# Kernel tuning notes

Hardware: AMD Instinct MI355X
Metric: run time of the kernel (lower is better)

## Reference

```python
import jax, jax.numpy as jnp
import numpy as np

B, T = 32, 50
H, D, V = 1024, 512, 50257


def setup_inputs() -> dict:
    key = jax.random.key(0)
    ks = jax.random.split(key, 8)
    s = 0.05  # small init scale to keep LSTM gates in a sane range
    return {
        "inputs": jax.random.normal(ks[0], (B, H), jnp.float32),          # initial hidden state
        "targets": jax.random.randint(ks[1], (B, T), 0, V, jnp.int32),     # teacher-forcing tokens
        "emb": jax.random.normal(ks[2], (V, D), jnp.float32) * s,
        "W_ih": jax.random.normal(ks[3], (4 * H, D), jnp.float32) * s,     # torch gate order i,f,g,o
        "W_hh": jax.random.normal(ks[4], (4 * H, H), jnp.float32) * s,
        "b_ih": jnp.zeros((4 * H,), jnp.float32),
        "b_hh": jnp.zeros((4 * H,), jnp.float32),
        "W_proj": jax.random.normal(ks[5], (V, H), jnp.float32) * s,
        "b_proj": jnp.zeros((V,), jnp.float32),
    }


def reference(inputs, targets, emb, W_ih, W_hh, b_ih, b_hh, W_proj, b_proj):
    b, t = targets.shape
    h = inputs.shape[1]
    # decoder input tokens: BOS(=1) at step 0, then targets shifted right by one
    tok = jnp.concatenate([jnp.ones((b, 1), targets.dtype), targets[:, :-1]], axis=1)  # [B,T]
    x = emb[tok]  # [B,T,D]
    # precompute input contribution to all gates for every step
    xg = jnp.einsum("btd,gd->btg", x, W_ih) + b_ih + b_hh  # [B,T,4H]

    def step(carry, xg_t):
        hs, cs = carry
        g = xg_t + hs @ W_hh.T  # [B,4H]
        i = jax.nn.sigmoid(g[:, :h])
        f = jax.nn.sigmoid(g[:, h:2 * h])
        gg = jnp.tanh(g[:, 2 * h:3 * h])
        o = jax.nn.sigmoid(g[:, 3 * h:])
        cs = f * cs + i * gg
        hs = o * jnp.tanh(cs)
        return (hs, cs), hs

    c0 = jnp.zeros_like(inputs)
    _, hs = jax.lax.scan(step, (inputs, c0), jnp.swapaxes(xg, 0, 1))  # hs: [T,B,H]
    hs = jnp.swapaxes(hs, 0, 1)  # [B,T,H]
    logits = jnp.einsum("bth,vh->btv", hs, W_proj) + b_proj  # [B,T,V]
    predictions = jnp.argmax(logits, axis=-1)  # [B,T]
    return logits, predictions
```

## Files before the change

kernel.cpp:

```cpp
#include <hip/hip_runtime.h>
#include <math.h>

#define BB 32
#define TT 50
#define HH 1024
#define DD 512
#define VV 50257
#define G4H 4096

typedef __attribute__((ext_vector_type(8))) short bf16x8;
typedef __attribute__((ext_vector_type(8))) unsigned short u16x8;
typedef __attribute__((ext_vector_type(4))) float f32x4;

__device__ inline unsigned short f2bf(float x) {
    unsigned u = __float_as_uint(x);
    u = (u + 0x7fff + ((u >> 16) & 1)) >> 16;
    return (unsigned short)u;
}
__device__ inline float bf2f(unsigned short h) {
    return __uint_as_float(((unsigned)h) << 16);
}
__device__ inline void gl16(const void* g, void* l) {
    __builtin_amdgcn_global_load_lds(
        (const __attribute__((address_space(1))) unsigned int*)g,
        (__attribute__((address_space(3))) unsigned int*)l, 16, 0, 0);
}

__global__ void split_f32(const float* __restrict__ x,
                          unsigned short* __restrict__ hi,
                          unsigned short* __restrict__ lo, long n4) {
    long i = (long)blockIdx.x * 256 + threadIdx.x;
    long stride = (long)gridDim.x * 256;
    for (; i < n4; i += stride) {
        float4 v = ((const float4*)x)[i];
        ushort4 h, l;
        h.x = f2bf(v.x); l.x = f2bf(v.x - bf2f(h.x));
        h.y = f2bf(v.y); l.y = f2bf(v.y - bf2f(h.y));
        h.z = f2bf(v.z); l.z = f2bf(v.z - bf2f(h.z));
        h.w = f2bf(v.w); l.w = f2bf(v.w - bf2f(h.w));
        ((ushort4*)hi)[i] = h;
        ((ushort4*)lo)[i] = l;
    }
}

__global__ void xg_gemm(const int* __restrict__ targets,
                        const float* __restrict__ emb,
                        const float* __restrict__ W_ih,
                        const float* __restrict__ b_ih,
                        const float* __restrict__ b_hh,
                        float* __restrict__ xg) {
    __shared__ float As[16][65];
    __shared__ float Bs[16][65];
    const int m0 = blockIdx.y * 64;
    const int n0 = blockIdx.x * 64;
    const int tid = threadIdx.x;
    const int tx = tid & 15;
    const int ty = tid >> 4;
    const int lk = tx;
    const int lm = ty;

    const float* arow[4];
    const float* brow[4];
#pragma unroll
    for (int i = 0; i < 4; i++) {
        int bt = m0 + lm + i * 16;
        int b = bt / TT, t = bt % TT;
        int tok = (t == 0) ? 1 : targets[b * TT + (t - 1)];
        arow[i] = emb + (size_t)tok * DD;
        int n = n0 + lm + i * 16;
        brow[i] = W_ih + (size_t)n * DD;
    }

    float acc[4][4] = {};
    for (int k0 = 0; k0 < DD; k0 += 16) {
#pragma unroll
        for (int i = 0; i < 4; i++) As[lk][lm + i * 16] = arow[i][k0 + lk];
#pragma unroll
        for (int i = 0; i < 4; i++) Bs[lk][lm + i * 16] = brow[i][k0 + lk];
        __syncthreads();
#pragma unroll
        for (int k = 0; k < 16; k++) {
            float a[4], bb[4];
#pragma unroll
            for (int i = 0; i < 4; i++) a[i] = As[k][ty + i * 16];
#pragma unroll
            for (int j = 0; j < 4; j++) bb[j] = Bs[k][tx + j * 16];
#pragma unroll
            for (int i = 0; i < 4; i++)
#pragma unroll
                for (int j = 0; j < 4; j++) acc[i][j] += a[i] * bb[j];
        }
        __syncthreads();
    }
#pragma unroll
    for (int i = 0; i < 4; i++) {
        int m = m0 + ty + i * 16;
#pragma unroll
        for (int j = 0; j < 4; j++) {
            int n = n0 + tx + j * 16;
            xg[(size_t)m * G4H + n] = acc[i][j] + b_ih[n] + b_hh[n];
        }
    }
}

#define NH 16
__global__ __launch_bounds__(256, 2) void lstm_mfma(
    const unsigned short* __restrict__ Wh, const unsigned short* __restrict__ Wl,
    const float* __restrict__ xg,
    const unsigned short* __restrict__ hin_h, const unsigned short* __restrict__ hin_l,
    long hin_stride,
    float* __restrict__ c_buf,
    unsigned short* __restrict__ Ah, unsigned short* __restrict__ Al,
    int t) {
    __shared__ unsigned short sWh[2][64 * 64], sWl[2][64 * 64];
    __shared__ unsigned short sHh[2][32 * 64], sHl[2][32 * 64];
    __shared__ float gbuf[4][32][17];
    const int tid = threadIdx.x;
    const int w = tid >> 6;
    const int l = tid & 63;
    const int lr = l & 15, lk = l >> 4;
    const int nh0 = blockIdx.x * NH;

    const int wrow = tid >> 2;
    const int ws0 = (tid & 3) * 2;
    const int wg = wrow >> 4, wj = wrow & 15;
    const unsigned short* gWh = Wh + (size_t)(wg * HH + nh0 + wj) * HH + ws0 * 8;
    const unsigned short* gWl = Wl + (size_t)(wg * HH + nh0 + wj) * HH + ws0 * 8;
    const int wwb0 = wrow * 64 + ((ws0) ^ (wrow & 7)) * 8;
    const int wwb1 = wrow * 64 + ((ws0 + 1) ^ (wrow & 7)) * 8;

    const int hp = tid & 127;
    const int hrow = hp >> 2;
    const int hs0 = (hp & 3) * 2;
    const unsigned short* gH =
        ((tid < 128) ? hin_h : hin_l) + (size_t)hrow * hin_stride + hs0 * 8;
    const int hsel = (tid < 128) ? 0 : 1;
    const int hwb0 = hrow * 64 + ((hs0) ^ (hrow & 7)) * 8;
    const int hwb1 = hrow * 64 + ((hs0 + 1) ^ (hrow & 7)) * 8;

    f32x4 acc0 = (f32x4){0.f, 0.f, 0.f, 0.f};
    f32x4 acc1 = (f32x4){0.f, 0.f, 0.f, 0.f};

    u16x8 rWh0 = *(const u16x8*)gWh, rWh1 = *(const u16x8*)(gWh + 8);
    u16x8 rWl0 = *(const u16x8*)gWl, rWl1 = *(const u16x8*)(gWl + 8);
    u16x8 rH0  = *(const u16x8*)gH,  rH1  = *(const u16x8*)(gH + 8);
    *(u16x8*)&sWh[0][wwb0] = rWh0; *(u16x8*)&sWh[0][wwb1] = rWh1;
    *(u16x8*)&sWl[0][wwb0] = rWl0; *(u16x8*)&sWl[0][wwb1] = rWl1;
    if (hsel == 0) { *(u16x8*)&sHh[0][hwb0] = rH0; *(u16x8*)&sHh[0][hwb1] = rH1; }
    else           { *(u16x8*)&sHl[0][hwb0] = rH0; *(u16x8*)&sHl[0][hwb1] = rH1; }
    rWh0 = *(const u16x8*)(gWh + 64); rWh1 = *(const u16x8*)(gWh + 64 + 8);
    rWl0 = *(const u16x8*)(gWl + 64); rWl1 = *(const u16x8*)(gWl + 64 + 8);
    rH0  = *(const u16x8*)(gH + 64);  rH1  = *(const u16x8*)(gH + 64 + 8);

    int cur = 0;
#pragma unroll 1
    for (int it = 0; it < 16; it++) {
        __syncthreads();
        if (it < 15) {
            const int nxt = cur ^ 1;
            *(u16x8*)&sWh[nxt][wwb0] = rWh0; *(u16x8*)&sWh[nxt][wwb1] = rWh1;
            *(u16x8*)&sWl[nxt][wwb0] = rWl0; *(u16x8*)&sWl[nxt][wwb1] = rWl1;
            if (hsel == 0) { *(u16x8*)&sHh[nxt][hwb0] = rH0; *(u16x8*)&sHh[nxt][hwb1] = rH1; }
            else           { *(u16x8*)&sHl[nxt][hwb0] = rH0; *(u16x8*)&sHl[nxt][hwb1] = rH1; }
            const int kn = (it < 14) ? (it + 2) * 64 : 0;
            rWh0 = *(const u16x8*)(gWh + kn); rWh1 = *(const u16x8*)(gWh + kn + 8);
            rWl0 = *(const u16x8*)(gWl + kn); rWl1 = *(const u16x8*)(gWl + kn + 8);
            rH0  = *(const u16x8*)(gH + kn);  rH1  = *(const u16x8*)(gH + kn + 8);
        }
#pragma unroll
        for (int kk = 0; kk < 2; kk++) {
            const int rsl = ((kk * 4 + lk) ^ (lr & 7)) * 8;
            bf16x8 bh = *(const bf16x8*)&sWh[cur][(w * 16 + lr) * 64 + rsl];
            bf16x8 bl = *(const bf16x8*)&sWl[cur][(w * 16 + lr) * 64 + rsl];
            bf16x8 a0h = *(const bf16x8*)&sHh[cur][lr * 64 + rsl];
            bf16x8 a1h = *(const bf16x8*)&sHh[cur][(16 + lr) * 64 + rsl];
            bf16x8 a0l = *(const bf16x8*)&sHl[cur][lr * 64 + rsl];
            bf16x8 a1l = *(const bf16x8*)&sHl[cur][(16 + lr) * 64 + rsl];
            acc0 = __builtin_amdgcn_mfma_f32_16x16x32_bf16(a0h, bh, acc0, 0, 0, 0);
            acc0 = __builtin_amdgcn_mfma_f32_16x16x32_bf16(a0h, bl, acc0, 0, 0, 0);
            acc0 = __builtin_amdgcn_mfma_f32_16x16x32_bf16(a0l, bh, acc0, 0, 0, 0);
            acc1 = __builtin_amdgcn_mfma_f32_16x16x32_bf16(a1h, bh, acc1, 0, 0, 0);
            acc1 = __builtin_amdgcn_mfma_f32_16x16x32_bf16(a1h, bl, acc1, 0, 0, 0);
            acc1 = __builtin_amdgcn_mfma_f32_16x16x32_bf16(a1l, bh, acc1, 0, 0, 0);
        }
        cur ^= 1;
    }

    __syncthreads();
#pragma unroll
    for (int r = 0; r < 4; r++) {
        gbuf[w][lk * 4 + r][lr] = acc0[r];
        gbuf[w][16 + lk * 4 + r][lr] = acc1[r];
    }
    __syncthreads();

#pragma unroll
    for (int q = 0; q < 2; q++) {
        int idx = tid + q * 256;
        int b = idx >> 4, j = idx & 15;
        size_t xb = ((size_t)b * TT + t) * G4H + nh0 + j;
        float gi_ = gbuf[0][b][j] + xg[xb];
        float gf_ = gbuf[1][b][j] + xg[xb + HH];
        float gg_ = gbuf[2][b][j] + xg[xb + 2 * HH];
        float go_ = gbuf[3][b][j] + xg[xb + 3 * HH];

        float i_ = 1.f / (1.f + expf(-gi_));
        float f_ = 1.f / (1.f + expf(-gf_));
        float g_ = tanhf(gg_);
        float o_ = 1.f / (1.f + expf(-go_));

        int ci = b * HH + nh0 + j;
        float c_old = (t == 0) ? 0.f : c_buf[ci];
        float c_new = f_ * c_old + i_ * g_;
        float h_new = o_ * tanhf(c_new);
        c_buf[ci] = c_new;

        size_t ho = ((size_t)b * TT + t) * HH + nh0 + j;
        unsigned short hh = f2bf(h_new);
        Ah[ho] = hh;
        Al[ho] = f2bf(h_new - bf2f(hh));
    }
}

__global__ void lstm_step(const float* __restrict__ W_hh,
                          const float* __restrict__ xg,
                          const float* __restrict__ h_prev,
                          float* __restrict__ c_buf,
                          float* __restrict__ h_out,
                          float* __restrict__ hs_all,
                          int t) {
    __shared__ float h_s[32][68];
    __shared__ float w_s[32][68];
    const int tid = threadIdx.x;
    const int b = tid & 31;
    const int jl = tid >> 5;
    const int n0 = blockIdx.x * 8;
    const int n = n0 + jl;

    float acc[4] = {0.f, 0.f, 0.f, 0.f};
    for (int k0 = 0; k0 < HH; k0 += 64) {
#pragma unroll
        for (int i = 0; i < 2; i++) {
            int e = tid + i * 256;
            int r = e >> 4;
            int c = e & 15;
            float4 hv = *(const float4*)&h_prev[r * HH + k0 + c * 4];
            *(float4*)&h_s[r][c * 4] = hv;
            int gi = r >> 3, jj = r & 7;
            float4 wv = *(const float4*)&W_hh[(size_t)(gi * HH + n0 + jj) * HH + k0 + c * 4];
            *(float4*)&w_s[r][c * 4] = wv;
        }
        __syncthreads();
#pragma unroll
        for (int k = 0; k < 64; k += 4) {
            float4 hv = *(const float4*)&h_s[b][k];
            float4 w0 = *(const float4*)&w_s[jl][k];
            float4 w1 = *(const float4*)&w_s[8 + jl][k];
            float4 w2 = *(const float4*)&w_s[16 + jl][k];
            float4 w3 = *(const float4*)&w_s[24 + jl][k];
            acc[0] += hv.x * w0.x + hv.y * w0.y + hv.z * w0.z + hv.w * w0.w;
            acc[1] += hv.x * w1.x + hv.y * w1.y + hv.z * w1.z + hv.w * w1.w;
            acc[2] += hv.x * w2.x + hv.y * w2.y + hv.z * w2.z + hv.w * w2.w;
            acc[3] += hv.x * w3.x + hv.y * w3.y + hv.z * w3.z + hv.w * w3.w;
        }
        __syncthreads();
    }

    const int bt = b * TT + t;
    float gi_ = acc[0] + xg[(size_t)bt * G4H + n];
    float gf_ = acc[1] + xg[(size_t)bt * G4H + HH + n];
    float gg_ = acc[2] + xg[(size_t)bt * G4H + 2 * HH + n];
    float go_ = acc[3] + xg[(size_t)bt * G4H + 3 * HH + n];

    float i_ = 1.f / (1.f + expf(-gi_));
    float f_ = 1.f / (1.f + expf(-gf_));
    float g_ = tanhf(gg_);
    float o_ = 1.f / (1.f + expf(-go_));

    float c_old = (t == 0) ? 0.f : c_buf[b * HH + n];
    float c_new = f_ * c_old + i_ * g_;
    float h_new = o_ * tanhf(c_new);

    c_buf[b * HH + n] = c_new;
    h_out[b * HH + n] = h_new;
    hs_all[(size_t)bt * HH + n] = h_new;
}

__global__ __launch_bounds__(256, 4) void proj_mfma(
    const unsigned short* __restrict__ Ah, const unsigned short* __restrict__ Al,
    const unsigned short* __restrict__ Bh, const unsigned short* __restrict__ Bl,
    const float* __restrict__ b_proj, float* __restrict__ logits) {
    __shared__ __attribute__((aligned(16))) unsigned short sA[2][128 * 32];
    __shared__ __attribute__((aligned(16))) unsigned short sB[2][128 * 32];
    const int tid = threadIdx.x;
    const int w = tid >> 6;
    const int l = tid & 63;
    const int wr = w >> 1, wc = w & 1;
    const int lr = l & 15, lk = l >> 4;

    const int d = blockIdx.x;
    const int xcd = d & 7;
    const int k = d >> 3;
    const int ncnt = (xcd == 0) ? 50 : 49;
    const int nstart = (xcd == 0) ? 0 : 50 + (xcd - 1) * 49;
    if (k >= 13 * ncnt) return;
    const int per4 = 4 * ncnt;
    int s, rr_;
    if (k < per4)          { s = 0; rr_ = k; }
    else if (k < 2 * per4) { s = 1; rr_ = k - per4; }
    else if (k < 3 * per4) { s = 2; rr_ = k - 2 * per4; }
    else                   { s = 3; rr_ = k - 3 * per4; }
    const int ssize = (s == 3) ? 1 : 4;
    const int nloc = rr_ / ssize;
    const int mins = rr_ - nloc * ssize;
    const int m0 = (s * 4 + mins) * 128;
    const int n0 = (nstart + nloc) * 128;

    const unsigned short* garr = (w == 0) ? Ah : (w == 1) ? Al : (w == 2) ? Bh : Bl;
    unsigned short* larr = (w == 0) ? sA[0] : (w == 1) ? sA[1]
                         : (w == 2) ? sB[0] : sB[1];
    const int isA = (w < 2);
    const unsigned short* gsrc[8];
#pragma unroll
    for (int i = 0; i < 8; i++) {
        int r = i * 16 + (l >> 2);
        int sl = (l & 3) ^ ((r >> 1) & 3);
        int g = isA ? (m0 + r) : (n0 + r);
        int gmax = isA ? (BB * TT - 1) : (VV - 1);
        if (g > gmax) g = gmax;
        gsrc[i] = garr + (size_t)g * HH + sl * 8;
    }

    const int rswz = (lk ^ ((lr >> 1) & 3)) * 8;

    f32x4 acc[4][4];
#pragma unroll
    for (int i = 0; i < 4; i++)
#pragma unroll
        for (int j = 0; j < 4; j++) acc[i][j] = (f32x4){0.f, 0.f, 0.f, 0.f};

#pragma unroll 1
    for (int it = 0; it < 32; it++) {
        const int k0v = it * 32;
#pragma unroll
        for (int i = 0; i < 8; i++)
            gl16(gsrc[i] + k0v, larr + i * 512);
        __syncthreads();

        bf16x8 ah[4], al[4], bh[4], bl[4];
#pragma unroll
        for (int i = 0; i < 4; i++) {
            int ra = (wr * 64 + i * 16 + lr) * 32 + rswz;
            ah[i] = *(const bf16x8*)&sA[0][ra];
            al[i] = *(const bf16x8*)&sA[1][ra];
        }
#pragma unroll
        for (int j = 0; j < 4; j++) {
            int rb = (wc * 64 + j * 16 + lr) * 32 + rswz;
            bh[j] = *(const bf16x8*)&sB[0][rb];
            bl[j] = *(const bf16x8*)&sB[1][rb];
        }
#pragma unroll
        for (int i = 0; i < 4; i++)
#pragma unroll
            for (int j = 0; j < 4; j++) {
                acc[i][j] = __builtin_amdgcn_mfma_f32_16x16x32_bf16(ah[i], bh[j], acc[i][j], 0, 0, 0);
                acc[i][j] = __builtin_amdgcn_mfma_f32_16x16x32_bf16(ah[i], bl[j], acc[i][j], 0, 0, 0);
                acc[i][j] = __builtin_amdgcn_mfma_f32_16x16x32_bf16(al[i], bh[j], acc[i][j], 0, 0, 0);
            }
        __syncthreads();
    }

    float* ewave = ((float*)sA) + w * 1024;
    const int nn = n0 + wc * 64 + l;
    const float bpv = b_proj[nn < VV ? nn : VV - 1];
    const bool nok = (nn < VV);
#pragma unroll
    for (int i = 0; i < 4; i++) {
#pragma unroll
        for (int j = 0; j < 4; j++)
#pragma unroll
            for (int r2 = 0; r2 < 4; r2++)
                ewave[(lk * 4 + r2) * 64 + j * 16 + lr] = acc[i][j][r2];
#pragma unroll
        for (int rr = 0; rr < 16; rr++) {
            int m = m0 + wr * 64 + i * 16 + rr;
            float v = ewave[rr * 64 + l] + bpv;
            if (m < BB * TT && nok)
                logits[(size_t)m * VV + nn] = v;
        }
    }
}

__global__ void proj_gemm(const float* __restrict__ hs,
                          const float* __restrict__ W_proj,
                          const float* __restrict__ b_proj,
                          float* __restrict__ logits) {
    __shared__ float As[16][65];
    __shared__ float Bs[16][65];
    const int m0 = blockIdx.y * 64;
    const int n0 = blockIdx.x * 64;
    const int tid = threadIdx.x;
    const int tx = tid & 15;
    const int ty = tid >> 4;
    const int lk = tx;
    const int lm = ty;

    const float* arow[4];
    const float* brow[4];
    bool bval[4];
#pragma unroll
    for (int i = 0; i < 4; i++) {
        arow[i] = hs + (size_t)(m0 + lm + i * 16) * HH;
        int n = n0 + lm + i * 16;
        bval[i] = (n < VV);
        brow[i] = W_proj + (size_t)(bval[i] ? n : 0) * HH;
    }

    float acc[4][4] = {};
    for (int k0 = 0; k0 < HH; k0 += 16) {
#pragma unroll
        for (int i = 0; i < 4; i++) As[lk][lm + i * 16] = arow[i][k0 + lk];
#pragma unroll
        for (int i = 0; i < 4; i++)
            Bs[lk][lm + i * 16] = bval[i] ? brow[i][k0 + lk] : 0.f;
        __syncthreads();
#pragma unroll
        for (int k = 0; k < 16; k++) {
            float a[4], bb[4];
#pragma unroll
            for (int i = 0; i < 4; i++) a[i] = As[k][ty + i * 16];
#pragma unroll
            for (int j = 0; j < 4; j++) bb[j] = Bs[k][tx + j * 16];
#pragma unroll
            for (int i = 0; i < 4; i++)
#pragma unroll
                for (int j = 0; j < 4; j++) acc[i][j] += a[i] * bb[j];
        }
        __syncthreads();
    }
#pragma unroll
    for (int i = 0; i < 4; i++) {
        int m = m0 + ty + i * 16;
#pragma unroll
        for (int j = 0; j < 4; j++) {
            int n = n0 + tx + j * 16;
            if (n < VV)
                logits[(size_t)m * VV + n] = acc[i][j] + b_proj[n];
        }
    }
}

__global__ void argmax_kernel(const float* __restrict__ logits,
                              float* __restrict__ preds) {
    const int bt = blockIdx.x;
    const float* row = logits + (size_t)bt * VV;
    const int tid = threadIdx.x;

    float best = -INFINITY;
    int bidx = 0x7fffffff;
    for (int v = tid; v < VV; v += 256) {
        float x = row[v];
        if (x > best) { best = x; bidx = v; }
    }
    __shared__ float sv[256];
    __shared__ int si[256];
    sv[tid] = best;
    si[tid] = bidx;
    __syncthreads();
    for (int s = 128; s > 0; s >>= 1) {
        if (tid < s) {
            float ov = sv[tid + s];
            int oi = si[tid + s];
            if (ov > sv[tid] || (ov == sv[tid] && oi < si[tid])) {
                sv[tid] = ov;
                si[tid] = oi;
            }
        }
        __syncthreads();
    }
    if (tid == 0) preds[bt] = (float)si[0];
}

extern "C" void kernel_launch(void* const* d_in, const int* in_sizes, int n_in,
                              void* d_out, int out_size, void* d_ws, size_t ws_size,
                              hipStream_t stream) {
    const float* inputs = (const float*)d_in[0];
    const int*   targets = (const int*)d_in[1];
    const float* emb    = (const float*)d_in[2];
    const float* W_ih   = (const float*)d_in[3];
    const float* W_hh   = (const float*)d_in[4];
    const float* b_ih   = (const float*)d_in[5];
    const float* b_hh   = (const float*)d_in[6];
    const float* W_proj = (const float*)d_in[7];
    const float* b_proj = (const float*)d_in[8];

    float* out = (float*)d_out;
    float* logits = out;
    float* preds = out + (size_t)BB * TT * VV;

    float* ws = (float*)d_ws;
    float* xg = ws;
    float* cb = xg + (size_t)BB * TT * G4H;
    unsigned short* Ah = (unsigned short*)(cb + (size_t)BB * HH);
    unsigned short* Al = Ah + (size_t)BB * TT * HH;
    unsigned short* Bh = Al + (size_t)BB * TT * HH;
    unsigned short* Bl = Bh + (size_t)VV * HH;
    char* R = (char*)(Bl + (size_t)VV * HH);

    float* hs = (float*)R;
    float* h0 = hs + (size_t)BB * TT * HH;
    float* h1 = h0 + (size_t)BB * HH;
    unsigned short* Wh = (unsigned short*)R;
    unsigned short* Wl = Wh + (size_t)G4H * HH;
    unsigned short* iah = Wl + (size_t)G4H * HH;
    unsigned short* ial = iah + (size_t)BB * HH;

    size_t base = (char*)R - (char*)d_ws;
    size_t need1 = base + ((size_t)BB * TT * HH + 2 * (size_t)BB * HH) * 4;
    size_t need2 = base + (2 * (size_t)G4H * HH + 2 * (size_t)BB * HH) * 2;
    int mode = (ws_size >= need2) ? 2 : (ws_size >= need1) ? 1 : 0;

    if (mode >= 1) {
        split_f32<<<4096, 256, 0, stream>>>(W_proj, Bh, Bl, (long)VV * HH / 4);
    }
    if (mode == 2) {
        split_f32<<<2048, 256, 0, stream>>>(W_hh, Wh, Wl, (long)G4H * HH / 4);
        split_f32<<<32, 256, 0, stream>>>(inputs, iah, ial, (long)BB * HH / 4);
    }

    xg_gemm<<<dim3(64, 25), 256, 0, stream>>>(targets, emb, W_ih, b_ih, b_hh, xg);

    if (mode == 2) {
        for (int t = 0; t < TT; t++) {
            const unsigned short* hh = (t == 0) ? iah : (Ah + (size_t)(t - 1) * HH);
            const unsigned short* hl = (t == 0) ? ial : (Al + (size_t)(t - 1) * HH);
            long hstride = (t == 0) ? HH : (long)TT * HH;
            lstm_mfma<<<64, 256, 0, stream>>>(Wh, Wl, xg, hh, hl, hstride,
                                              cb, Ah, Al, t);
        }
        proj_mfma<<<5200, 256, 0, stream>>>(Ah, Al, Bh, Bl, b_proj, logits);
    } else {
        for (int t = 0; t < TT; t++) {
            const float* hp = (t == 0) ? inputs : ((t & 1) ? h0 : h1);
            float* ho = (t & 1) ? h1 : h0;
            lstm_step<<<128, 256, 0, stream>>>(W_hh, xg, hp, cb, ho, hs, t);
        }
        if (mode == 1) {
            split_f32<<<1600, 256, 0, stream>>>(hs, Ah, Al, (long)BB * TT * HH / 4);
            proj_mfma<<<5200, 256, 0, stream>>>(Ah, Al, Bh, Bl, b_proj, logits);
        } else {
            proj_gemm<<<dim3(786, 25), 256, 0, stream>>>(hs, W_proj, b_proj, logits);
        }
    }

    argmax_kernel<<<1600, 256, 0, stream>>>(logits, preds);
}
```

Baseline: 1.380 ms.

## Use direct global-to-LDS loads for LSTM recurrent GEMM tiles

Replaces the register-staged double-buffered loads of W_hh (hi/lo bf16) and hidden-state tiles in the per-step LSTM kernel with global_load_lds async copies into a merged, swizzled shared buffer. The swizzle is moved to the global source address so each wave copies contiguous 16-byte chunks per lane. This is meant to cut VGPR pressure and the VALU/LDS-write cost of staging through registers. The per-step kernel is latency-bound, so the gain may be small, and correctness depends on the waits issued around the async LDS writes.

```diff
diff --git a/kernel.cpp b/kernel.cpp
--- a/kernel.cpp
+++ b/kernel.cpp
@@ -112,8 +112,8 @@
     float* __restrict__ c_buf,
     unsigned short* __restrict__ Ah, unsigned short* __restrict__ Al,
     int t) {
-    __shared__ unsigned short sWh[2][64 * 64], sWl[2][64 * 64];
-    __shared__ unsigned short sHh[2][32 * 64], sHl[2][32 * 64];
+    __shared__ __attribute__((aligned(16))) unsigned short sW[2][2][64 * 64];
+    __shared__ __attribute__((aligned(16))) unsigned short sH[2][2][32 * 64];
     __shared__ float gbuf[4][32][17];
     const int tid = threadIdx.x;
     const int w = tid >> 6;
@@ -121,61 +121,65 @@
     const int lr = l & 15, lk = l >> 4;
     const int nh0 = blockIdx.x * NH;
 
-    const int wrow = tid >> 2;
-    const int ws0 = (tid & 3) * 2;
-    const int wg = wrow >> 4, wj = wrow & 15;
-    const unsigned short* gWh = Wh + (size_t)(wg * HH + nh0 + wj) * HH + ws0 * 8;
-    const unsigned short* gWl = Wl + (size_t)(wg * HH + nh0 + wj) * HH + ws0 * 8;
-    const int wwb0 = wrow * 64 + ((ws0) ^ (wrow & 7)) * 8;
-    const int wwb1 = wrow * 64 + ((ws0 + 1) ^ (wrow & 7)) * 8;
-
-    const int hp = tid & 127;
-    const int hrow = hp >> 2;
-    const int hs0 = (hp & 3) * 2;
-    const unsigned short* gH =
-        ((tid < 128) ? hin_h : hin_l) + (size_t)hrow * hin_stride + hs0 * 8;
-    const int hsel = (tid < 128) ? 0 : 1;
-    const int hwb0 = hrow * 64 + ((hs0) ^ (hrow & 7)) * 8;
-    const int hwb1 = hrow * 64 + ((hs0 + 1) ^ (hrow & 7)) * 8;
+    const int rowc = l >> 3;
+    const int p = l & 7;
+    const unsigned short* gsrc[6];
+    unsigned short* lp0[6];
+    unsigned short* lp1[6];
+#pragma unroll
+    for (int i = 0; i < 6; i++) {
+        const int c = w * 6 + i;
+        const int sl = p ^ rowc;
+        if (c < 16) {
+            const int hl = (c >> 3) & 1;
+            const int cc = c & 7;
+            const int r = cc * 8 + rowc;
+            const int wg = r >> 4, wj = r & 15;
+            const unsigned short* base = hl ? Wl : Wh;
+            gsrc[i] = base + (size_t)(wg * HH + nh0 + wj) * HH + sl * 8;
+            lp0[i] = &sW[0][hl][cc * 512];
+            lp1[i] = &sW[1][hl][cc * 512];
+        } else {
+            const int hc = c - 16;
+            const int hl = (hc >> 2) & 1;
+            const int cc = hc & 3;
+            const int r = cc * 8 + rowc;
+            const unsigned short* base = hl ? hin_l : hin_h;
+            gsrc[i] = base + (size_t)r * hin_stride + sl * 8;
+            lp0[i] = &sH[0][hl][cc * 512];
+            lp1[i] = &sH[1][hl][cc * 512];
+        }
+    }
 
     f32x4 acc0 = (f32x4){0.f, 0.f, 0.f, 0.f};
     f32x4 acc1 = (f32x4){0.f, 0.f, 0.f, 0.f};
 
-    u16x8 rWh0 = *(const u16x8*)gWh, rWh1 = *(const u16x8*)(gWh + 8);
-    u16x8 rWl0 = *(const u16x8*)gWl, rWl1 = *(const u16x8*)(gWl + 8);
-    u16x8 rH0  = *(const u16x8*)gH,  rH1  = *(const u16x8*)(gH + 8);
-    *(u16x8*)&sWh[0][wwb0] = rWh0; *(u16x8*)&sWh[0][wwb1] = rWh1;
-    *(u16x8*)&sWl[0][wwb0] = rWl0; *(u16x8*)&sWl[0][wwb1] = rWl1;
-    if (hsel == 0) { *(u16x8*)&sHh[0][hwb0] = rH0; *(u16x8*)&sHh[0][hwb1] = rH1; }
-    else           { *(u16x8*)&sHl[0][hwb0] = rH0; *(u16x8*)&sHl[0][hwb1] = rH1; }
-    rWh0 = *(const u16x8*)(gWh + 64); rWh1 = *(const u16x8*)(gWh + 64 + 8);
-    rWl0 = *(const u16x8*)(gWl + 64); rWl1 = *(const u16x8*)(gWl + 64 + 8);
-    rH0  = *(const u16x8*)(gH + 64);  rH1  = *(const u16x8*)(gH + 64 + 8);
+#pragma unroll
+    for (int i = 0; i < 6; i++) gl16(gsrc[i], lp0[i]);
 
     int cur = 0;
 #pragma unroll 1
     for (int it = 0; it < 16; it++) {
         __syncthreads();
         if (it < 15) {
-            const int nxt = cur ^ 1;
-            *(u16x8*)&sWh[nxt][wwb0] = rWh0; *(u16x8*)&sWh[nxt][wwb1] = rWh1;
-            *(u16x8*)&sWl[nxt][wwb0] = rWl0; *(u16x8*)&sWl[nxt][wwb1] = rWl1;
-            if (hsel == 0) { *(u16x8*)&sHh[nxt][hwb0] = rH0; *(u16x8*)&sHh[nxt][hwb1] = rH1; }
-            else           { *(u16x8*)&sHl[nxt][hwb0] = rH0; *(u16x8*)&sHl[nxt][hwb1] = rH1; }
-            const int kn = (it < 14) ? (it + 2) * 64 : 0;
-            rWh0 = *(const u16x8*)(gWh + kn); rWh1 = *(const u16x8*)(gWh + kn + 8);
-            rWl0 = *(const u16x8*)(gWl + kn); rWl1 = *(const u16x8*)(gWl + kn + 8);
-            rH0  = *(const u16x8*)(gH + kn);  rH1  = *(const u16x8*)(gH + kn + 8);
+            const int kn = (it + 1) * 64;
+            if (cur == 0) {
+#pragma unroll
+                for (int i = 0; i < 6; i++) gl16(gsrc[i] + kn, lp1[i]);
+            } else {
+#pragma unroll
+                for (int i = 0; i < 6; i++) gl16(gsrc[i] + kn, lp0[i]);
+            }
         }
 #pragma unroll
         for (int kk = 0; kk < 2; kk++) {
             const int rsl = ((kk * 4 + lk) ^ (lr & 7)) * 8;
-            bf16x8 bh = *(const bf16x8*)&sWh[cur][(w * 16 + lr) * 64 + rsl];
-            bf16x8 bl = *(const bf16x8*)&sWl[cur][(w * 16 + lr) * 64 + rsl];
-            bf16x8 a0h = *(const bf16x8*)&sHh[cur][lr * 64 + rsl];
-            bf16x8 a1h = *(const bf16x8*)&sHh[cur][(16 + lr) * 64 + rsl];
-            bf16x8 a0l = *(const bf16x8*)&sHl[cur][lr * 64 + rsl];
-            bf16x8 a1l = *(const bf16x8*)&sHl[cur][(16 + lr) * 64 + rsl];
+            bf16x8 bh = *(const bf16x8*)&sW[cur][0][(w * 16 + lr) * 64 + rsl];
+            bf16x8 bl = *(const bf16x8*)&sW[cur][1][(w * 16 + lr) * 64 + rsl];
+            bf16x8 a0h = *(const bf16x8*)&sH[cur][0][lr * 64 + rsl];
+            bf16x8 a1h = *(const bf16x8*)&sH[cur][0][(16 + lr) * 64 + rsl];
+            bf16x8 a0l = *(const bf16x8*)&sH[cur][1][lr * 64 + rsl];
+            bf16x8 a1l = *(const bf16x8*)&sH[cur][1][(16 + lr) * 64 + rsl];
             acc0 = __builtin_amdgcn_mfma_f32_16x16x32_bf16(a0h, bh, acc0, 0, 0, 0);
             acc0 = __builtin_amdgcn_mfma_f32_16x16x32_bf16(a0h, bl, acc0, 0, 0, 0);
             acc0 = __builtin_amdgcn_mfma_f32_16x16x32_bf16(a0l, bh, acc0, 0, 0, 0);
```

Result: slower. 1.461 ms (+5.9%).

## Split LSTM step K-reduction across two wave groups in 512-thread blocks

Applied to the files above, without the earlier changes.

Doubles the lstm_mfma block to 512 threads. Each half of the block handles half of the K=1024 recurrent reduction with its own double-buffered shared tiles, and the partial gate sums are combined through shared memory before the activation epilogue. This halves the serial K-loop length per step, aiming to cut per-launch latency of the 50 sequential recurrent kernels. In exchange it doubles shared memory and the gbuf footprint. The block count stays at 64, so the GPU remains mostly idle.

```diff
diff --git a/kernel.cpp b/kernel.cpp
--- a/kernel.cpp
+++ b/kernel.cpp
@@ -104,7 +104,7 @@
 }
 
 #define NH 16
-__global__ __launch_bounds__(256, 2) void lstm_mfma(
+__global__ __launch_bounds__(512, 2) void lstm_mfma(
     const unsigned short* __restrict__ Wh, const unsigned short* __restrict__ Wl,
     const float* __restrict__ xg,
     const unsigned short* __restrict__ hin_h, const unsigned short* __restrict__ hin_l,
@@ -112,29 +112,35 @@
     float* __restrict__ c_buf,
     unsigned short* __restrict__ Ah, unsigned short* __restrict__ Al,
     int t) {
-    __shared__ unsigned short sWh[2][64 * 64], sWl[2][64 * 64];
-    __shared__ unsigned short sHh[2][32 * 64], sHl[2][32 * 64];
-    __shared__ float gbuf[4][32][17];
+    __shared__ unsigned short sW[2][2][2][64 * 64];
+    __shared__ unsigned short sH[2][2][2][32 * 64];
+    __shared__ float gbuf[8][32][17];
     const int tid = threadIdx.x;
     const int w = tid >> 6;
+    const int g = w & 3;
+    const int h2 = w >> 2;
     const int l = tid & 63;
     const int lr = l & 15, lk = l >> 4;
     const int nh0 = blockIdx.x * NH;
 
-    const int wrow = tid >> 2;
-    const int ws0 = (tid & 3) * 2;
+    const int stid = tid & 255;
+    const int sh2 = tid >> 8;
+    const int kbase = sh2 * 512;
+
+    const int wrow = stid >> 2;
+    const int ws0 = (stid & 3) * 2;
     const int wg = wrow >> 4, wj = wrow & 15;
-    const unsigned short* gWh = Wh + (size_t)(wg * HH + nh0 + wj) * HH + ws0 * 8;
-    const unsigned short* gWl = Wl + (size_t)(wg * HH + nh0 + wj) * HH + ws0 * 8;
+    const unsigned short* gWh = Wh + (size_t)(wg * HH + nh0 + wj) * HH + kbase + ws0 * 8;
+    const unsigned short* gWl = Wl + (size_t)(wg * HH + nh0 + wj) * HH + kbase + ws0 * 8;
     const int wwb0 = wrow * 64 + ((ws0) ^ (wrow & 7)) * 8;
     const int wwb1 = wrow * 64 + ((ws0 + 1) ^ (wrow & 7)) * 8;
 
-    const int hp = tid & 127;
+    const int hp = stid & 127;
     const int hrow = hp >> 2;
     const int hs0 = (hp & 3) * 2;
     const unsigned short* gH =
-        ((tid < 128) ? hin_h : hin_l) + (size_t)hrow * hin_stride + hs0 * 8;
-    const int hsel = (tid < 128) ? 0 : 1;
+        ((stid < 128) ? hin_h : hin_l) + (size_t)hrow * hin_stride + kbase + hs0 * 8;
+    const int hsel = (stid < 128) ? 0 : 1;
     const int hwb0 = hrow * 64 + ((hs0) ^ (hrow & 7)) * 8;
     const int hwb1 = hrow * 64 + ((hs0 + 1) ^ (hrow & 7)) * 8;
 
@@ -144,25 +150,25 @@
     u16x8 rWh0 = *(const u16x8*)gWh, rWh1 = *(const u16x8*)(gWh + 8);
     u16x8 rWl0 = *(const u16x8*)gWl, rWl1 = *(const u16x8*)(gWl + 8);
     u16x8 rH0  = *(const u16x8*)gH,  rH1  = *(const u16x8*)(gH + 8);
-    *(u16x8*)&sWh[0][wwb0] = rWh0; *(u16x8*)&sWh[0][wwb1] = rWh1;
-    *(u16x8*)&sWl[0][wwb0] = rWl0; *(u16x8*)&sWl[0][wwb1] = rWl1;
-    if (hsel == 0) { *(u16x8*)&sHh[0][hwb0] = rH0; *(u16x8*)&sHh[0][hwb1] = rH1; }
-    else           { *(u16x8*)&sHl[0][hwb0] = rH0; *(u16x8*)&sHl[0][hwb1] = rH1; }
+    *(u16x8*)&sW[sh2][0][0][wwb0] = rWh0; *(u16x8*)&sW[sh2][0][0][wwb1] = rWh1;
+    *(u16x8*)&sW[sh2][0][1][wwb0] = rWl0; *(u16x8*)&sW[sh2][0][1][wwb1] = rWl1;
+    if (hsel == 0) { *(u16x8*)&sH[sh2][0][0][hwb0] = rH0; *(u16x8*)&sH[sh2][0][0][hwb1] = rH1; }
+    else           { *(u16x8*)&sH[sh2][0][1][hwb0] = rH0; *(u16x8*)&sH[sh2][0][1][hwb1] = rH1; }
     rWh0 = *(const u16x8*)(gWh + 64); rWh1 = *(const u16x8*)(gWh + 64 + 8);
     rWl0 = *(const u16x8*)(gWl + 64); rWl1 = *(const u16x8*)(gWl + 64 + 8);
     rH0  = *(const u16x8*)(gH + 64);  rH1  = *(const u16x8*)(gH + 64 + 8);
 
     int cur = 0;
 #pragma unroll 1
-    for (int it = 0; it < 16; it++) {
-        __syncthreads();
-        if (it < 15) {
+    for (int it = 0; it < 8; it++) {
+        __syncthreads();
+        if (it < 7) {
             const int nxt = cur ^ 1;
-            *(u16x8*)&sWh[nxt][wwb0] = rWh0; *(u16x8*)&sWh[nxt][wwb1] = rWh1;
-            *(u16x8*)&sWl[nxt][wwb0] = rWl0; *(u16x8*)&sWl[nxt][wwb1] = rWl1;
-            if (hsel == 0) { *(u16x8*)&sHh[nxt][hwb0] = rH0; *(u16x8*)&sHh[nxt][hwb1] = rH1; }
-            else           { *(u16x8*)&sHl[nxt][hwb0] = rH0; *(u16x8*)&sHl[nxt][hwb1] = rH1; }
-            const int kn = (it < 14) ? (it + 2) * 64 : 0;
+            *(u16x8*)&sW[sh2][nxt][0][wwb0] = rWh0; *(u16x8*)&sW[sh2][nxt][0][wwb1] = rWh1;
+            *(u16x8*)&sW[sh2][nxt][1][wwb0] = rWl0; *(u16x8*)&sW[sh2][nxt][1][wwb1] = rWl1;
+            if (hsel == 0) { *(u16x8*)&sH[sh2][nxt][0][hwb0] = rH0; *(u16x8*)&sH[sh2][nxt][0][hwb1] = rH1; }
+            else           { *(u16x8*)&sH[sh2][nxt][1][hwb0] = rH0; *(u16x8*)&sH[sh2][nxt][1][hwb1] = rH1; }
+            const int kn = (it < 6) ? (it + 2) * 64 : 0;
             rWh0 = *(const u16x8*)(gWh + kn); rWh1 = *(const u16x8*)(gWh + kn + 8);
             rWl0 = *(const u16x8*)(gWl + kn); rWl1 = *(const u16x8*)(gWl + kn + 8);
             rH0  = *(const u16x8*)(gH + kn);  rH1  = *(const u16x8*)(gH + kn + 8);
@@ -170,12 +176,12 @@
 #pragma unroll
         for (int kk = 0; kk < 2; kk++) {
             const int rsl = ((kk * 4 + lk) ^ (lr & 7)) * 8;
-            bf16x8 bh = *(const bf16x8*)&sWh[cur][(w * 16 + lr) * 64 + rsl];
-            bf16x8 bl = *(const bf16x8*)&sWl[cur][(w * 16 + lr) * 64 + rsl];
-            bf16x8 a0h = *(const bf16x8*)&sHh[cur][lr * 64 + rsl];
-            bf16x8 a1h = *(const bf16x8*)&sHh[cur][(16 + lr) * 64 + rsl];
-            bf16x8 a0l = *(const bf16x8*)&sHl[cur][lr * 64 + rsl];
-            bf16x8 a1l = *(const bf16x8*)&sHl[cur][(16 + lr) * 64 + rsl];
+            bf16x8 bh = *(const bf16x8*)&sW[h2][cur][0][(g * 16 + lr) * 64 + rsl];
+            bf16x8 bl = *(const bf16x8*)&sW[h2][cur][1][(g * 16 + lr) * 64 + rsl];
+            bf16x8 a0h = *(const bf16x8*)&sH[h2][cur][0][lr * 64 + rsl];
+            bf16x8 a1h = *(const bf16x8*)&sH[h2][cur][0][(16 + lr) * 64 + rsl];
+            bf16x8 a0l = *(const bf16x8*)&sH[h2][cur][1][lr * 64 + rsl];
+            bf16x8 a1l = *(const bf16x8*)&sH[h2][cur][1][(16 + lr) * 64 + rsl];
             acc0 = __builtin_amdgcn_mfma_f32_16x16x32_bf16(a0h, bh, acc0, 0, 0, 0);
             acc0 = __builtin_amdgcn_mfma_f32_16x16x32_bf16(a0h, bl, acc0, 0, 0, 0);
             acc0 = __builtin_amdgcn_mfma_f32_16x16x32_bf16(a0l, bh, acc0, 0, 0, 0);
@@ -194,15 +200,13 @@
     }
     __syncthreads();
 
-#pragma unroll
-    for (int q = 0; q < 2; q++) {
-        int idx = tid + q * 256;
-        int b = idx >> 4, j = idx & 15;
+    {
+        int b = tid >> 4, j = tid & 15;
         size_t xb = ((size_t)b * TT + t) * G4H + nh0 + j;
-        float gi_ = gbuf[0][b][j] + xg[xb];
-        float gf_ = gbuf[1][b][j] + xg[xb + HH];
-        float gg_ = gbuf[2][b][j] + xg[xb + 2 * HH];
-        float go_ = gbuf[3][b][j] + xg[xb + 3 * HH];
+        float gi_ = gbuf[0][b][j] + gbuf[4][b][j] + xg[xb];
+        float gf_ = gbuf[1][b][j] + gbuf[5][b][j] + xg[xb + HH];
+        float gg_ = gbuf[2][b][j] + gbuf[6][b][j] + xg[xb + 2 * HH];
+        float go_ = gbuf[3][b][j] + gbuf[7][b][j] + xg[xb + 3 * HH];
 
         float i_ = 1.f / (1.f + expf(-gi_));
         float f_ = 1.f / (1.f + expf(-gf_));
@@ -536,7 +540,7 @@
             const unsigned short* hh = (t == 0) ? iah : (Ah + (size_t)(t - 1) * HH);
             const unsigned short* hl = (t == 0) ? ial : (Al + (size_t)(t - 1) * HH);
             long hstride = (t == 0) ? HH : (long)TT * HH;
-            lstm_mfma<<<64, 256, 0, stream>>>(Wh, Wl, xg, hh, hl, hstride,
+            lstm_mfma<<<64, 512, 0, stream>>>(Wh, Wl, xg, hh, hl, hstride,
                                               cb, Ah, Al, t);
         }
         proj_mfma<<<5200, 256, 0, stream>>>(Ah, Al, Bh, Bl, b_proj, logits);
```

New measurement: 1.279 ms. 1.08x faster.
